# Performance work log

Measured on AMD Instinct MI355X. Metric: run time of the kernel, lower is better.

## Reference

```python
import jax, jax.numpy as jnp
import numpy as np

D_MODEL = 1024
N_HEADS = 16
HEAD_DIM = D_MODEL // N_HEADS
SCALE = HEAD_DIM ** (-0.5)
D_GRAPH = 8
B, N = 4, 1024
NEG_INF = -1.0e9


def setup_inputs() -> dict:
    key = jax.random.key(0)
    ks = jax.random.split(key, 8)
    std = (2.0 / (5.0 * D_MODEL)) ** 0.5
    q = jax.random.normal(ks[0], (B, N, D_MODEL), dtype=jnp.float32)
    k = jax.random.normal(ks[1], (B, N, D_MODEL), dtype=jnp.float32)
    v = jax.random.normal(ks[2], (B, N, D_MODEL), dtype=jnp.float32)
    mask = jax.random.randint(ks[3], (B, N), 0, 2).astype(bool)
    graphormer_dists = jax.random.uniform(ks[4], (B, N, N, D_GRAPH), dtype=jnp.float32)
    weights = std * jax.random.normal(ks[5], (4 * D_MODEL, D_MODEL), dtype=jnp.float32)
    biases = jnp.zeros((4 * D_MODEL,), dtype=jnp.float32)
    w_graph = std * jax.random.normal(ks[6], (N_HEADS, D_GRAPH), dtype=jnp.float32)
    return {"q": q, "k": k, "v": v, "mask": mask,
            "graphormer_dists": graphormer_dists,
            "weights": weights, "biases": biases, "w_graph": w_graph}


def _proj(x, weights, biases, start, end):
    # F.linear with a slice of the fused [4*d_model, d_model] weight
    return x @ weights[start:end].T + biases[start:end]


def _split_heads(x):
    b, n, _ = x.shape
    return x.reshape(b, n, N_HEADS, HEAD_DIM).transpose(0, 2, 1, 3)  # bhnd


def reference(q, k, v, mask, graphormer_dists, weights, biases, w_graph):
    b, n, _ = q.shape
    qh = _split_heads(_proj(q, weights, biases, 0, D_MODEL))
    kh = _split_heads(_proj(k, weights, biases, D_MODEL, 2 * D_MODEL))
    vh = _split_heads(_proj(v, weights, biases, 2 * D_MODEL, 3 * D_MODEL))
    # dot-product scores, scaled
    att = jnp.einsum('bhnd,bhmd->bhnm', qh, kh) * SCALE
    # graphormer bias: Linear(d_graph -> n_heads), then permute to bhnm
    att = att + jnp.einsum('bnmp,hp->bhnm', graphormer_dists, w_graph)
    # mask fills along the QUERY dim (mask[:,None,:,None]), as in the source
    att = jnp.where(mask[:, None, :, None], NEG_INF, att)
    att = jax.nn.softmax(att, axis=-1)
    # dropout p=0.0 (eval): identity
    out = jnp.einsum('bhnm,bhmd->bhnd', att, vh)
    out = out.transpose(0, 2, 1, 3).reshape(b, n, D_MODEL)
    out = _proj(out, weights, biases, 3 * D_MODEL, 4 * D_MODEL)
    return out, att
```

## Files before the change

### kernel.cpp

```cpp
#include <hip/hip_runtime.h>
#include <hip/hip_bf16.h>

#define SEQ      1024
#define BATCH    4
#define NHEADS   16
#define HDIM     64
#define DMODEL   1024
#define DGRAPH   8
#define QK_SCALE 0.125f
#define PCONST   0.0009765625f

typedef __attribute__((ext_vector_type(8))) short bf16x8;
typedef __attribute__((ext_vector_type(4))) float f32x4;

__device__ __forceinline__ void split_bf16(float x, short& hi, short& lo) {
    unsigned u = __float_as_uint(x);
    hi = (short)(u >> 16);
    float hf = __uint_as_float(u & 0xffff0000u);
    lo = (short)(__float_as_uint(x - hf) >> 16);
}

__global__ void zero_f32(float* p, int n) {
    int i = blockIdx.x * 256 + threadIdx.x;
    if (i < n) p[i] = 0.f;
}

template<int OUTMODE>
__global__ __launch_bounds__(256) void proj_mfma(
    const float* __restrict__ X,
    const float* __restrict__ W,
    const float* __restrict__ bias,
    float* __restrict__ Yf,
    short* __restrict__ Yhi,
    short* __restrict__ Ylo,
    float scale)
{
    constexpr int LDK = 40;
    __shared__ short Ah[128 * LDK];
    __shared__ short Al[128 * LDK];
    __shared__ short Bh[64 * LDK];
    __shared__ short Bl[64 * LDK];

    const int t   = threadIdx.x;
    const int w   = t >> 6;
    const int l   = t & 63;
    const int l15 = l & 15;
    const int lk  = (l >> 4) * 8;
    const int m0  = blockIdx.y * 128;
    const int c0  = blockIdx.x * 64;
    const int wr  = (w >> 1) * 64;
    const int wc  = (w & 1) * 32;

    const int srow = t >> 2;
    const int skg  = t & 3;

    f32x4 acc[4][2];
#pragma unroll
    for (int i = 0; i < 4; ++i)
#pragma unroll
        for (int j = 0; j < 2; ++j) acc[i][j] = f32x4{0.f, 0.f, 0.f, 0.f};

    float xa[2][8];
    float wa[8];

#pragma unroll
    for (int i = 0; i < 2; ++i) {
        const float* p = X + (size_t)(m0 + srow + i * 64) * DMODEL + skg * 8;
        float4 u0 = *(const float4*)p;
        float4 u1 = *(const float4*)(p + 4);
        xa[i][0] = u0.x; xa[i][1] = u0.y; xa[i][2] = u0.z; xa[i][3] = u0.w;
        xa[i][4] = u1.x; xa[i][5] = u1.y; xa[i][6] = u1.z; xa[i][7] = u1.w;
    }
    {
        const float* p = W + (size_t)(c0 + srow) * DMODEL + skg * 8;
        float4 u0 = *(const float4*)p;
        float4 u1 = *(const float4*)(p + 4);
        wa[0] = u0.x; wa[1] = u0.y; wa[2] = u0.z; wa[3] = u0.w;
        wa[4] = u1.x; wa[5] = u1.y; wa[6] = u1.z; wa[7] = u1.w;
    }

    for (int kt = 0; kt < 32; ++kt) {
#pragma unroll
        for (int i = 0; i < 2; ++i) {
            bf16x8 hv, lv;
#pragma unroll
            for (int j = 0; j < 8; ++j) {
                short h, s; split_bf16(xa[i][j], h, s);
                hv[j] = h; lv[j] = s;
            }
            *(bf16x8*)(Ah + (srow + i * 64) * LDK + skg * 8) = hv;
            *(bf16x8*)(Al + (srow + i * 64) * LDK + skg * 8) = lv;
        }
        {
            bf16x8 hv, lv;
#pragma unroll
            for (int j = 0; j < 8; ++j) {
                short h, s; split_bf16(wa[j], h, s);
                hv[j] = h; lv[j] = s;
            }
            *(bf16x8*)(Bh + srow * LDK + skg * 8) = hv;
            *(bf16x8*)(Bl + srow * LDK + skg * 8) = lv;
        }
        __syncthreads();

        if (kt + 1 < 32) {
            const int k0 = (kt + 1) * 32;
#pragma unroll
            for (int i = 0; i < 2; ++i) {
                const float* p = X + (size_t)(m0 + srow + i * 64) * DMODEL + k0 + skg * 8;
                float4 u0 = *(const float4*)p;
                float4 u1 = *(const float4*)(p + 4);
                xa[i][0] = u0.x; xa[i][1] = u0.y; xa[i][2] = u0.z; xa[i][3] = u0.w;
                xa[i][4] = u1.x; xa[i][5] = u1.y; xa[i][6] = u1.z; xa[i][7] = u1.w;
            }
            const float* p = W + (size_t)(c0 + srow) * DMODEL + k0 + skg * 8;
            float4 u0 = *(const float4*)p;
            float4 u1 = *(const float4*)(p + 4);
            wa[0] = u0.x; wa[1] = u0.y; wa[2] = u0.z; wa[3] = u0.w;
            wa[4] = u1.x; wa[5] = u1.y; wa[6] = u1.z; wa[7] = u1.w;
        }

        bf16x8 ah[4], alo[4], bh[2], blo[2];
#pragma unroll
        for (int fm = 0; fm < 4; ++fm) {
            const int off = (wr + fm * 16 + l15) * LDK + lk;
            ah[fm]  = *(const bf16x8*)(Ah + off);
            alo[fm] = *(const bf16x8*)(Al + off);
        }
#pragma unroll
        for (int fn = 0; fn < 2; ++fn) {
            const int off = (wc + fn * 16 + l15) * LDK + lk;
            bh[fn]  = *(const bf16x8*)(Bh + off);
            blo[fn] = *(const bf16x8*)(Bl + off);
        }
#pragma unroll
        for (int fm = 0; fm < 4; ++fm)
#pragma unroll
            for (int fn = 0; fn < 2; ++fn) {
                acc[fm][fn] = __builtin_amdgcn_mfma_f32_16x16x32_bf16(
                    ah[fm], bh[fn], acc[fm][fn], 0, 0, 0);
                acc[fm][fn] = __builtin_amdgcn_mfma_f32_16x16x32_bf16(
                    ah[fm], blo[fn], acc[fm][fn], 0, 0, 0);
                acc[fm][fn] = __builtin_amdgcn_mfma_f32_16x16x32_bf16(
                    alo[fm], bh[fn], acc[fm][fn], 0, 0, 0);
            }
        __syncthreads();
    }

#pragma unroll
    for (int fm = 0; fm < 4; ++fm)
#pragma unroll
        for (int fn = 0; fn < 2; ++fn) {
            const int c = c0 + wc + fn * 16 + l15;
            const float bb = bias[c];
#pragma unroll
            for (int r = 0; r < 4; ++r) {
                const int m = m0 + wr + fm * 16 + (l >> 4) * 4 + r;
                const float v = (acc[fm][fn][r] + bb) * scale;
                if constexpr (OUTMODE == 0) {
                    Yf[(size_t)m * DMODEL + c] = v;
                } else {
                    const int b_ = m >> 10, n = m & 1023;
                    const int h = c >> 6, d = c & 63;
                    const size_t idx =
                        ((size_t)((b_ * NHEADS + h) * SEQ + n)) * HDIM + d;
                    if constexpr (OUTMODE == 1) {
                        Yf[idx] = v;
                    } else {
                        short hi, lo; split_bf16(v, hi, lo);
                        Yhi[idx] = hi; Ylo[idx] = lo;
                    }
                }
            }
        }
}

__global__ __launch_bounds__(256) void graph_bias_kernel(
    const float* __restrict__ dists,
    const float* __restrict__ wg,
    const int* __restrict__ mask,
    float* __restrict__ attL)
{
    const int n = blockIdx.x & 1023;
    const int b = blockIdx.x >> 10;
    if (mask[b * SEQ + n]) return;

    __shared__ float wgs[NHEADS * DGRAPH];
    const int t = threadIdx.x;
    if (t < NHEADS * DGRAPH) wgs[t] = wg[t];
    __syncthreads();

    const int m = t * 4;
    const float* dp = dists + (((size_t)(b * SEQ + n)) * SEQ + m) * DGRAPH;
    float d[4][8];
#pragma unroll
    for (int i = 0; i < 8; ++i) {
        float4 v = *reinterpret_cast<const float4*>(dp + i * 4);
        d[i >> 1][(i & 1) * 4 + 0] = v.x; d[i >> 1][(i & 1) * 4 + 1] = v.y;
        d[i >> 1][(i & 1) * 4 + 2] = v.z; d[i >> 1][(i & 1) * 4 + 3] = v.w;
    }
#pragma unroll
    for (int h = 0; h < NHEADS; ++h) {
        float ov[4];
#pragma unroll
        for (int jm = 0; jm < 4; ++jm) {
            float s = 0.f;
#pragma unroll
            for (int p = 0; p < DGRAPH; ++p)
                s = fmaf(d[jm][p], wgs[h * DGRAPH + p], s);
            ov[jm] = s;
        }
        float4 o; o.x = ov[0]; o.y = ov[1]; o.z = ov[2]; o.w = ov[3];
        *reinterpret_cast<float4*>(
            attL + (((size_t)((b * NHEADS + h) * SEQ + n)) * SEQ + m)) = o;
    }
}

__global__ __launch_bounds__(256) void qk_mfma(
    const short* __restrict__ Qhi, const short* __restrict__ Qlo,
    const short* __restrict__ Khi, const short* __restrict__ Klo,
    const int* __restrict__ mask,
    float* __restrict__ attL,
    float* __restrict__ rowSum)
{
    constexpr int LDK = 72;
    __shared__ short sQh[128 * LDK];
    __shared__ short sQl[128 * LDK];
    __shared__ short sKh[128 * LDK];
    __shared__ short sKl[128 * LDK];
    __shared__ int maskS[128];

    const int t   = threadIdx.x;
    const int w   = t >> 6;
    const int l   = t & 63;
    const int l15 = l & 15;
    const int lk  = (l >> 4) * 8;
    const int m0  = blockIdx.x * 128;
    const int n0  = blockIdx.y * 128;
    const int bh  = blockIdx.z;
    const int b   = bh >> 4;

    if (t < 128) maskS[t] = mask[b * SEQ + n0 + t];

#pragma unroll
    for (int it = 0; it < 4; ++it) {
        const int f   = t + it * 256;
        const int row = f >> 3;
        const int c8  = f & 7;
        const size_t gq = ((size_t)bh * SEQ + n0 + row) * HDIM + c8 * 8;
        const size_t gk = ((size_t)bh * SEQ + m0 + row) * HDIM + c8 * 8;
        const int lo = row * LDK + c8 * 8;
        *(bf16x8*)(sQh + lo) = *(const bf16x8*)(Qhi + gq);
        *(bf16x8*)(sQl + lo) = *(const bf16x8*)(Qlo + gq);
        *(bf16x8*)(sKh + lo) = *(const bf16x8*)(Khi + gk);
        *(bf16x8*)(sKl + lo) = *(const bf16x8*)(Klo + gk);
    }

    const int nr = (w >> 1) * 64;
    const int mc = (w & 1) * 64;

    f32x4 acc[4][4];
    {
        const float* bb = attL + ((size_t)bh * SEQ + n0 + nr + (l >> 4) * 4) * SEQ
                          + m0 + mc + l15;
#pragma unroll
        for (int fm = 0; fm < 4; ++fm)
#pragma unroll
            for (int fn = 0; fn < 4; ++fn)
#pragma unroll
                for (int r = 0; r < 4; ++r)
                    acc[fm][fn][r] = bb[(size_t)(fm * 16 + r) * SEQ + fn * 16];
    }
    __syncthreads();

#pragma unroll
    for (int ks = 0; ks < 2; ++ks) {
        bf16x8 ah[4], alo[4], bhv[4], blo[4];
#pragma unroll
        for (int fm = 0; fm < 4; ++fm) {
            const int off = (nr + fm * 16 + l15) * LDK + ks * 32 + lk;
            ah[fm]  = *(const bf16x8*)(sQh + off);
            alo[fm] = *(const bf16x8*)(sQl + off);
        }
#pragma unroll
        for (int fn = 0; fn < 4; ++fn) {
            const int off = (mc + fn * 16 + l15) * LDK + ks * 32 + lk;
            bhv[fn] = *(const bf16x8*)(sKh + off);
            blo[fn] = *(const bf16x8*)(sKl + off);
        }
#pragma unroll
        for (int fm = 0; fm < 4; ++fm)
#pragma unroll
            for (int fn = 0; fn < 4; ++fn) {
                acc[fm][fn] = __builtin_amdgcn_mfma_f32_16x16x32_bf16(
                    ah[fm], bhv[fn], acc[fm][fn], 0, 0, 0);
                acc[fm][fn] = __builtin_amdgcn_mfma_f32_16x16x32_bf16(
                    ah[fm], blo[fn], acc[fm][fn], 0, 0, 0);
                acc[fm][fn] = __builtin_amdgcn_mfma_f32_16x16x32_bf16(
                    alo[fm], bhv[fn], acc[fm][fn], 0, 0, 0);
            }
    }

#pragma unroll
    for (int fm = 0; fm < 4; ++fm)
#pragma unroll
        for (int r = 0; r < 4; ++r) {
            const int nloc = nr + fm * 16 + (l >> 4) * 4 + r;
            const bool msk = maskS[nloc] != 0;
            float* rowp = attL + ((size_t)bh * SEQ + n0 + nloc) * SEQ + m0 + mc + l15;
            float s = 0.f;
#pragma unroll
            for (int fn = 0; fn < 4; ++fn) {
                const float e = __expf(acc[fm][fn][r]);
                s += e;
                if (!msk) rowp[fn * 16] = e;
            }
            s += __shfl_xor(s, 1); s += __shfl_xor(s, 2);
            s += __shfl_xor(s, 4); s += __shfl_xor(s, 8);
            if (!msk && l15 == 0)
                atomicAdd(rowSum + (size_t)bh * SEQ + n0 + nloc, s);
        }
}

__global__ __launch_bounds__(256) void softmax_pv_kernel(
    float* __restrict__ attL,
    const float* __restrict__ VH,
    const int* __restrict__ mask,
    const float* __restrict__ rowSum,
    float* __restrict__ AO)
{
    __shared__ float pS[128 * 32];
    __shared__ float Vs[32][68];
    __shared__ float rowInv[128];
    __shared__ int   maskS[128];

    const int t    = threadIdx.x;
    const int n0   = blockIdx.x * 128;
    const int h    = blockIdx.y;
    const int b    = blockIdx.z;
    const int bh   = b * NHEADS + h;
    float* Lbase = attL + ((size_t)bh * SEQ + n0) * SEQ;

    if (t < 128) {
        const int mk = mask[b * SEQ + n0 + t];
        maskS[t] = mk;
        rowInv[t] = mk ? 0.f : 1.0f / rowSum[(size_t)bh * SEQ + n0 + t];
    }
    __syncthreads();

    const int TX = t & 7;
    const int TY = t >> 3;
    float acc[4][8];
#pragma unroll
    for (int i = 0; i < 4; ++i)
#pragma unroll
        for (int d = 0; d < 8; ++d) acc[i][d] = 0.f;

    float4 sreg[4];
#pragma unroll
    for (int i = 0; i < 4; ++i) sreg[i] = make_float4(0.f, 0.f, 0.f, 0.f);

#pragma unroll
    for (int i = 0; i < 4; ++i) {
        int f4 = t + i * 256;
        int row = f4 >> 3, mq = f4 & 7;
        if (!maskS[row])
            sreg[i] = *reinterpret_cast<const float4*>(
                Lbase + (size_t)row * SEQ + mq * 4);
    }

    for (int mc = 0; mc < 32; ++mc) {
#pragma unroll
        for (int i = 0; i < 4; ++i) {
            int f4 = t + i * 256;
            int row = f4 >> 3, mq = f4 & 7;
            float4 p4;
            if (maskS[row]) {
                p4.x = PCONST; p4.y = PCONST; p4.z = PCONST; p4.w = PCONST;
            } else {
                const float iv = rowInv[row];
                p4.x = sreg[i].x * iv;
                p4.y = sreg[i].y * iv;
                p4.z = sreg[i].z * iv;
                p4.w = sreg[i].w * iv;
            }
            *reinterpret_cast<float4*>(
                Lbase + (size_t)row * SEQ + mc * 32 + mq * 4) = p4;
            *reinterpret_cast<float4*>(
                pS + row * 32 + ((mq ^ ((row >> 3) & 7)) << 2)) = p4;
        }
#pragma unroll
        for (int i = 0; i < 2; ++i) {
            int f4 = t + i * 256;
            int m = f4 >> 4, dq = f4 & 15;
            *reinterpret_cast<float4*>(&Vs[m][dq * 4]) =
                *reinterpret_cast<const float4*>(
                    VH + ((size_t)bh * SEQ + mc * 32 + m) * HDIM + dq * 4);
        }
        __syncthreads();

        if (mc + 1 < 32) {
#pragma unroll
            for (int i = 0; i < 4; ++i) {
                int f4 = t + i * 256;
                int row = f4 >> 3, mq = f4 & 7;
                if (!maskS[row])
                    sreg[i] = *reinterpret_cast<const float4*>(
                        Lbase + (size_t)row * SEQ + (mc + 1) * 32 + mq * 4);
            }
        }

#pragma unroll
        for (int m4 = 0; m4 < 8; ++m4) {
            float pav[4][4];
#pragma unroll
            for (int i = 0; i < 4; ++i) {
                int row = TY * 4 + i;
                float4 p = *reinterpret_cast<const float4*>(
                    pS + row * 32 + ((m4 ^ ((row >> 3) & 7)) << 2));
                pav[i][0] = p.x; pav[i][1] = p.y; pav[i][2] = p.z; pav[i][3] = p.w;
            }
#pragma unroll
            for (int j = 0; j < 4; ++j) {
                float4 v0 = *reinterpret_cast<const float4*>(&Vs[m4 * 4 + j][TX * 8]);
                float4 v1 = *reinterpret_cast<const float4*>(&Vs[m4 * 4 + j][TX * 8 + 4]);
                float vb[8] = {v0.x, v0.y, v0.z, v0.w, v1.x, v1.y, v1.z, v1.w};
#pragma unroll
                for (int i = 0; i < 4; ++i)
#pragma unroll
                    for (int d = 0; d < 8; ++d)
                        acc[i][d] = fmaf(pav[i][j], vb[d], acc[i][d]);
            }
        }
        __syncthreads();
    }

#pragma unroll
    for (int i = 0; i < 4; ++i) {
        int n = n0 + TY * 4 + i;
        float4 o0, o1;
        o0.x = acc[i][0]; o0.y = acc[i][1]; o0.z = acc[i][2]; o0.w = acc[i][3];
        o1.x = acc[i][4]; o1.y = acc[i][5]; o1.z = acc[i][6]; o1.w = acc[i][7];
        float* op = AO + ((size_t)(b * SEQ + n)) * DMODEL + h * HDIM + TX * 8;
        *reinterpret_cast<float4*>(op)     = o0;
        *reinterpret_cast<float4*>(op + 4) = o1;
    }
}

extern "C" void kernel_launch(void* const* d_in, const int* in_sizes, int n_in,
                              void* d_out, int out_size, void* d_ws, size_t ws_size,
                              hipStream_t stream) {
    const float* q       = (const float*)d_in[0];
    const float* k       = (const float*)d_in[1];
    const float* v       = (const float*)d_in[2];
    const int*   mask    = (const int*)d_in[3];
    const float* dists   = (const float*)d_in[4];
    const float* weights = (const float*)d_in[5];
    const float* biases  = (const float*)d_in[6];
    const float* wg      = (const float*)d_in[7];

    float* out  = (float*)d_out;
    float* attL = out + (size_t)BATCH * SEQ * DMODEL;

    const size_t HSZ = (size_t)BATCH * NHEADS * SEQ * HDIM;
    short* Qhi = (short*)d_ws;
    short* Qlo = Qhi + HSZ;
    short* Khi = Qlo + HSZ;
    short* Klo = Khi + HSZ;
    float* VH  = (float*)(Klo + HSZ);
    float* AO  = (float*)d_ws;
    float* rowSum = out;

    const int NROWS = BATCH * NHEADS * SEQ;
    zero_f32<<<(NROWS + 255) / 256, 256, 0, stream>>>(rowSum, NROWS);

    dim3 gProj(DMODEL / 64, (BATCH * SEQ) / 128);
    proj_mfma<2><<<gProj, 256, 0, stream>>>(q, weights, biases,
                                            nullptr, Qhi, Qlo, QK_SCALE);
    proj_mfma<2><<<gProj, 256, 0, stream>>>(k, weights + 1 * (size_t)DMODEL * DMODEL,
                                            biases + DMODEL, nullptr, Khi, Klo, 1.0f);
    proj_mfma<1><<<gProj, 256, 0, stream>>>(v, weights + 2 * (size_t)DMODEL * DMODEL,
                                            biases + 2 * DMODEL, VH, nullptr, nullptr, 1.0f);

    graph_bias_kernel<<<BATCH * SEQ, 256, 0, stream>>>(dists, wg, mask, attL);

    dim3 gQK(SEQ / 128, SEQ / 128, BATCH * NHEADS);
    qk_mfma<<<gQK, 256, 0, stream>>>(Qhi, Qlo, Khi, Klo, mask, attL, rowSum);

    dim3 gPV(SEQ / 128, NHEADS, BATCH);
    softmax_pv_kernel<<<gPV, 256, 0, stream>>>(attL, VH, mask, rowSum, AO);

    proj_mfma<0><<<gProj, 256, 0, stream>>>(AO, weights + 3 * (size_t)DMODEL * DMODEL,
                                            biases + 3 * DMODEL, out, nullptr, nullptr, 1.0f);
}
```

Before: 476.8 us.

## Move P·V onto MFMA with split-bf16 and transposed V projection output

Replaces the scalar-FMA softmax·V kernel with an MFMA version that splits P and V into hi/lo bf16 pairs and runs three MFMAs per tile, and widens the key chunk to 64. The V projection now writes transposed hi/lo bf16 so V tiles load contiguously along the sequence. The QK kernel also skips loading the graph bias for masked query rows. This aims to cut the FP32 ALU cost of the PV matmul, at the cost of extra split/convert work and slight precision loss from the bf16x3 emulation.

```diff
diff --git a/kernel.cpp b/kernel.cpp
--- a/kernel.cpp
+++ b/kernel.cpp
@@ -11,6 +11,7 @@
 #define PCONST   0.0009765625f
 
 typedef __attribute__((ext_vector_type(8))) short bf16x8;
+typedef __attribute__((ext_vector_type(4))) short bf16x4;
 typedef __attribute__((ext_vector_type(4))) float f32x4;
 
 __device__ __forceinline__ void split_bf16(float x, short& hi, short& lo) {
@@ -162,12 +163,14 @@
                 } else {
                     const int b_ = m >> 10, n = m & 1023;
                     const int h = c >> 6, d = c & 63;
-                    const size_t idx =
-                        ((size_t)((b_ * NHEADS + h) * SEQ + n)) * HDIM + d;
-                    if constexpr (OUTMODE == 1) {
-                        Yf[idx] = v;
+                    short hi, lo; split_bf16(v, hi, lo);
+                    if constexpr (OUTMODE == 2) {
+                        const size_t idx =
+                            ((size_t)((b_ * NHEADS + h) * SEQ + n)) * HDIM + d;
+                        Yhi[idx] = hi; Ylo[idx] = lo;
                     } else {
-                        short hi, lo; split_bf16(v, hi, lo);
+                        const size_t idx =
+                            ((size_t)((b_ * NHEADS + h) * HDIM + d)) * SEQ + n;
                         Yhi[idx] = hi; Ylo[idx] = lo;
                     }
                 }
@@ -255,6 +258,7 @@
         *(bf16x8*)(sKh + lo) = *(const bf16x8*)(Khi + gk);
         *(bf16x8*)(sKl + lo) = *(const bf16x8*)(Klo + gk);
     }
+    __syncthreads();
 
     const int nr = (w >> 1) * 64;
     const int mc = (w & 1) * 64;
@@ -266,12 +270,15 @@
 #pragma unroll
         for (int fm = 0; fm < 4; ++fm)
 #pragma unroll
-            for (int fn = 0; fn < 4; ++fn)
-#pragma unroll
-                for (int r = 0; r < 4; ++r)
-                    acc[fm][fn][r] = bb[(size_t)(fm * 16 + r) * SEQ + fn * 16];
-    }
-    __syncthreads();
+            for (int r = 0; r < 4; ++r) {
+                const int nloc = nr + fm * 16 + (l >> 4) * 4 + r;
+                const bool mk = maskS[nloc] != 0;
+#pragma unroll
+                for (int fn = 0; fn < 4; ++fn)
+                    acc[fm][fn][r] =
+                        mk ? 0.f : bb[(size_t)(fm * 16 + r) * SEQ + fn * 16];
+            }
+    }
 
 #pragma unroll
     for (int ks = 0; ks < 2; ++ks) {
@@ -322,23 +329,31 @@
         }
 }
 
-__global__ __launch_bounds__(256) void softmax_pv_kernel(
+__global__ __launch_bounds__(256) void pv_mfma(
     float* __restrict__ attL,
-    const float* __restrict__ VH,
+    const short* __restrict__ VThi,
+    const short* __restrict__ VTlo,
     const int* __restrict__ mask,
     const float* __restrict__ rowSum,
     float* __restrict__ AO)
 {
-    __shared__ float pS[128 * 32];
-    __shared__ float Vs[32][68];
+    constexpr int LDP = 72;
+    __shared__ short pHi[128 * LDP];
+    __shared__ short pLo[128 * LDP];
+    __shared__ short sVh[64 * LDP];
+    __shared__ short sVl[64 * LDP];
     __shared__ float rowInv[128];
     __shared__ int   maskS[128];
 
-    const int t    = threadIdx.x;
-    const int n0   = blockIdx.x * 128;
-    const int h    = blockIdx.y;
-    const int b    = blockIdx.z;
-    const int bh   = b * NHEADS + h;
+    const int t   = threadIdx.x;
+    const int w   = t >> 6;
+    const int l   = t & 63;
+    const int l15 = l & 15;
+    const int lk  = (l >> 4) * 8;
+    const int n0  = blockIdx.x * 128;
+    const int h   = blockIdx.y;
+    const int b   = blockIdx.z;
+    const int bh  = b * NHEADS + h;
     float* Lbase = attL + ((size_t)bh * SEQ + n0) * SEQ;
 
     if (t < 128) {
@@ -348,103 +363,114 @@
     }
     __syncthreads();
 
-    const int TX = t & 7;
-    const int TY = t >> 3;
-    float acc[4][8];
+    const int nr = (w >> 1) * 64;
+    const int dc = (w & 1) * 32;
+
+    f32x4 acc[4][2];
 #pragma unroll
     for (int i = 0; i < 4; ++i)
 #pragma unroll
-        for (int d = 0; d < 8; ++d) acc[i][d] = 0.f;
-
-    float4 sreg[4];
-#pragma unroll
-    for (int i = 0; i < 4; ++i) sreg[i] = make_float4(0.f, 0.f, 0.f, 0.f);
-
-#pragma unroll
-    for (int i = 0; i < 4; ++i) {
-        int f4 = t + i * 256;
-        int row = f4 >> 3, mq = f4 & 7;
+        for (int j = 0; j < 2; ++j) acc[i][j] = f32x4{0.f, 0.f, 0.f, 0.f};
+
+    float4 sreg[8];
+#pragma unroll
+    for (int i = 0; i < 8; ++i) sreg[i] = make_float4(0.f, 0.f, 0.f, 0.f);
+#pragma unroll
+    for (int i = 0; i < 8; ++i) {
+        const int f4 = t + i * 256;
+        const int row = f4 >> 4, mq = f4 & 15;
         if (!maskS[row])
             sreg[i] = *reinterpret_cast<const float4*>(
                 Lbase + (size_t)row * SEQ + mq * 4);
     }
 
-    for (int mc = 0; mc < 32; ++mc) {
-#pragma unroll
-        for (int i = 0; i < 4; ++i) {
-            int f4 = t + i * 256;
-            int row = f4 >> 3, mq = f4 & 7;
+    for (int mc = 0; mc < 16; ++mc) {
+#pragma unroll
+        for (int i = 0; i < 8; ++i) {
+            const int f4 = t + i * 256;
+            const int row = f4 >> 4, mq = f4 & 15;
             float4 p4;
             if (maskS[row]) {
                 p4.x = PCONST; p4.y = PCONST; p4.z = PCONST; p4.w = PCONST;
             } else {
                 const float iv = rowInv[row];
-                p4.x = sreg[i].x * iv;
-                p4.y = sreg[i].y * iv;
-                p4.z = sreg[i].z * iv;
-                p4.w = sreg[i].w * iv;
+                p4.x = sreg[i].x * iv; p4.y = sreg[i].y * iv;
+                p4.z = sreg[i].z * iv; p4.w = sreg[i].w * iv;
             }
             *reinterpret_cast<float4*>(
-                Lbase + (size_t)row * SEQ + mc * 32 + mq * 4) = p4;
-            *reinterpret_cast<float4*>(
-                pS + row * 32 + ((mq ^ ((row >> 3) & 7)) << 2)) = p4;
+                Lbase + (size_t)row * SEQ + mc * 64 + mq * 4) = p4;
+            bf16x4 hv, lv;
+            short h0, s0, h1, s1, h2, s2, h3, s3;
+            split_bf16(p4.x, h0, s0); split_bf16(p4.y, h1, s1);
+            split_bf16(p4.z, h2, s2); split_bf16(p4.w, h3, s3);
+            hv[0] = h0; hv[1] = h1; hv[2] = h2; hv[3] = h3;
+            lv[0] = s0; lv[1] = s1; lv[2] = s2; lv[3] = s3;
+            *(bf16x4*)(pHi + row * LDP + mq * 4) = hv;
+            *(bf16x4*)(pLo + row * LDP + mq * 4) = lv;
         }
 #pragma unroll
         for (int i = 0; i < 2; ++i) {
-            int f4 = t + i * 256;
-            int m = f4 >> 4, dq = f4 & 15;
-            *reinterpret_cast<float4*>(&Vs[m][dq * 4]) =
-                *reinterpret_cast<const float4*>(
-                    VH + ((size_t)bh * SEQ + mc * 32 + m) * HDIM + dq * 4);
+            const int f = t + i * 256;
+            const int d = f >> 3, m8 = f & 7;
+            const size_t src = ((size_t)bh * HDIM + d) * SEQ + mc * 64 + m8 * 8;
+            *(bf16x8*)(sVh + d * LDP + m8 * 8) = *(const bf16x8*)(VThi + src);
+            *(bf16x8*)(sVl + d * LDP + m8 * 8) = *(const bf16x8*)(VTlo + src);
         }
         __syncthreads();
 
-        if (mc + 1 < 32) {
-#pragma unroll
-            for (int i = 0; i < 4; ++i) {
-                int f4 = t + i * 256;
-                int row = f4 >> 3, mq = f4 & 7;
+        if (mc + 1 < 16) {
+#pragma unroll
+            for (int i = 0; i < 8; ++i) {
+                const int f4 = t + i * 256;
+                const int row = f4 >> 4, mq = f4 & 15;
                 if (!maskS[row])
                     sreg[i] = *reinterpret_cast<const float4*>(
-                        Lbase + (size_t)row * SEQ + (mc + 1) * 32 + mq * 4);
-            }
-        }
-
-#pragma unroll
-        for (int m4 = 0; m4 < 8; ++m4) {
-            float pav[4][4];
-#pragma unroll
-            for (int i = 0; i < 4; ++i) {
-                int row = TY * 4 + i;
-                float4 p = *reinterpret_cast<const float4*>(
-                    pS + row * 32 + ((m4 ^ ((row >> 3) & 7)) << 2));
-                pav[i][0] = p.x; pav[i][1] = p.y; pav[i][2] = p.z; pav[i][3] = p.w;
-            }
-#pragma unroll
-            for (int j = 0; j < 4; ++j) {
-                float4 v0 = *reinterpret_cast<const float4*>(&Vs[m4 * 4 + j][TX * 8]);
-                float4 v1 = *reinterpret_cast<const float4*>(&Vs[m4 * 4 + j][TX * 8 + 4]);
-                float vb[8] = {v0.x, v0.y, v0.z, v0.w, v1.x, v1.y, v1.z, v1.w};
-#pragma unroll
-                for (int i = 0; i < 4; ++i)
-#pragma unroll
-                    for (int d = 0; d < 8; ++d)
-                        acc[i][d] = fmaf(pav[i][j], vb[d], acc[i][d]);
-            }
+                        Lbase + (size_t)row * SEQ + (mc + 1) * 64 + mq * 4);
+            }
+        }
+
+#pragma unroll
+        for (int ks = 0; ks < 2; ++ks) {
+            bf16x8 ah[4], alo[4], bhv[2], blo[2];
+#pragma unroll
+            for (int fm = 0; fm < 4; ++fm) {
+                const int off = (nr + fm * 16 + l15) * LDP + ks * 32 + lk;
+                ah[fm]  = *(const bf16x8*)(pHi + off);
+                alo[fm] = *(const bf16x8*)(pLo + off);
+            }
+#pragma unroll
+            for (int fn = 0; fn < 2; ++fn) {
+                const int off = (dc + fn * 16 + l15) * LDP + ks * 32 + lk;
+                bhv[fn] = *(const bf16x8*)(sVh + off);
+                blo[fn] = *(const bf16x8*)(sVl + off);
+            }
+#pragma unroll
+            for (int fm = 0; fm < 4; ++fm)
+#pragma unroll
+                for (int fn = 0; fn < 2; ++fn) {
+                    acc[fm][fn] = __builtin_amdgcn_mfma_f32_16x16x32_bf16(
+                        ah[fm], bhv[fn], acc[fm][fn], 0, 0, 0);
+                    acc[fm][fn] = __builtin_amdgcn_mfma_f32_16x16x32_bf16(
+                        ah[fm], blo[fn], acc[fm][fn], 0, 0, 0);
+                    acc[fm][fn] = __builtin_amdgcn_mfma_f32_16x16x32_bf16(
+                        alo[fm], bhv[fn], acc[fm][fn], 0, 0, 0);
+                }
         }
         __syncthreads();
     }
 
 #pragma unroll
-    for (int i = 0; i < 4; ++i) {
-        int n = n0 + TY * 4 + i;
-        float4 o0, o1;
-        o0.x = acc[i][0]; o0.y = acc[i][1]; o0.z = acc[i][2]; o0.w = acc[i][3];
-        o1.x = acc[i][4]; o1.y = acc[i][5]; o1.z = acc[i][6]; o1.w = acc[i][7];
-        float* op = AO + ((size_t)(b * SEQ + n)) * DMODEL + h * HDIM + TX * 8;
-        *reinterpret_cast<float4*>(op)     = o0;
-        *reinterpret_cast<float4*>(op + 4) = o1;
-    }
+    for (int fm = 0; fm < 4; ++fm)
+#pragma unroll
+        for (int fn = 0; fn < 2; ++fn) {
+            const int dd = dc + fn * 16 + l15;
+#pragma unroll
+            for (int r = 0; r < 4; ++r) {
+                const int n = n0 + nr + fm * 16 + (l >> 4) * 4 + r;
+                AO[((size_t)(b * SEQ + n)) * DMODEL + h * HDIM + dd] =
+                    acc[fm][fn][r];
+            }
+        }
 }
 
 extern "C" void kernel_launch(void* const* d_in, const int* in_sizes, int n_in,
@@ -463,12 +489,13 @@
     float* attL = out + (size_t)BATCH * SEQ * DMODEL;
 
     const size_t HSZ = (size_t)BATCH * NHEADS * SEQ * HDIM;
-    short* Qhi = (short*)d_ws;
-    short* Qlo = Qhi + HSZ;
-    short* Khi = Qlo + HSZ;
-    short* Klo = Khi + HSZ;
-    float* VH  = (float*)(Klo + HSZ);
-    float* AO  = (float*)d_ws;
+    short* Qhi  = (short*)d_ws;
+    short* Qlo  = Qhi + HSZ;
+    short* Khi  = Qlo + HSZ;
+    short* Klo  = Khi + HSZ;
+    short* VThi = Klo + HSZ;
+    short* VTlo = VThi + HSZ;
+    float* AO   = (float*)d_ws;
     float* rowSum = out;
 
     const int NROWS = BATCH * NHEADS * SEQ;
@@ -479,8 +506,8 @@
                                             nullptr, Qhi, Qlo, QK_SCALE);
     proj_mfma<2><<<gProj, 256, 0, stream>>>(k, weights + 1 * (size_t)DMODEL * DMODEL,
                                             biases + DMODEL, nullptr, Khi, Klo, 1.0f);
-    proj_mfma<1><<<gProj, 256, 0, stream>>>(v, weights + 2 * (size_t)DMODEL * DMODEL,
-                                            biases + 2 * DMODEL, VH, nullptr, nullptr, 1.0f);
+    proj_mfma<3><<<gProj, 256, 0, stream>>>(v, weights + 2 * (size_t)DMODEL * DMODEL,
+                                            biases + 2 * DMODEL, nullptr, VThi, VTlo, 1.0f);
 
     graph_bias_kernel<<<BATCH * SEQ, 256, 0, stream>>>(dists, wg, mask, attL);
 
@@ -488,7 +515,7 @@
     qk_mfma<<<gQK, 256, 0, stream>>>(Qhi, Qlo, Khi, Klo, mask, attL, rowSum);
 
     dim3 gPV(SEQ / 128, NHEADS, BATCH);
-    softmax_pv_kernel<<<gPV, 256, 0, stream>>>(attL, VH, mask, rowSum, AO);
+    pv_mfma<<<gPV, 256, 0, stream>>>(attL, VThi, VTlo, mask, rowSum, AO);
 
     proj_mfma<0><<<gProj, 256, 0, stream>>>(AO, weights + 3 * (size_t)DMODEL * DMODEL,
                                             biases + 3 * DMODEL, out, nullptr, nullptr, 1.0f);
```

Measured after the change: 437.8 us. 8.2% less time.
